# Kernel optimization log

Measured on AMD Instinct MI355X. Metric: run time of the kernel, lower is better.

The kernel has to match this reference:

```python
import jax, jax.numpy as jnp
import numpy as np

B, T, N, M, L = 128, 1024, 256, 256, 2
SCALE = 1.0 / np.sqrt(M)  # PyTorch uniform(-1/sqrt(m), 1/sqrt(m)) stdev-ish scale


def setup_inputs() -> dict:
    key = jax.random.key(0)
    ks = jax.random.split(key, 9)
    inp = {"X": jax.random.normal(ks[0], (B, T, N), dtype=jnp.float32)}
    names = ["w_ih_0", "w_hh_0", "b_ih_0", "b_hh_0", "w_ih_1", "w_hh_1", "b_ih_1", "b_hh_1"]
    shapes = [(3 * M, N), (3 * M, M), (3 * M,), (3 * M,), (3 * M, M), (3 * M, M), (3 * M,), (3 * M,)]
    for name, shp, k in zip(names, shapes, ks[1:]):
        inp[name] = jax.random.normal(k, shp, dtype=jnp.float32) * SCALE
    return inp


def _gru_layer(x, w_ih, w_hh, b_ih, b_hh):
    # x: [B, T, in] ; weights: [3m, in], [3m, m] ; gate order r, z, n (PyTorch)
    b, t, _ = x.shape
    m = w_hh.shape[1]
    gates_x = jnp.einsum('bti,gi->btg', x, w_ih) + b_ih  # [B, T, 3m], precomputed input gates

    def step(h, gx):
        gh = h @ w_hh.T + b_hh  # [B, 3m]
        r = jax.nn.sigmoid(gx[:, :m] + gh[:, :m])
        z = jax.nn.sigmoid(gx[:, m:2 * m] + gh[:, m:2 * m])
        n = jnp.tanh(gx[:, 2 * m:] + r * gh[:, 2 * m:])
        h_new = (1.0 - z) * n + z * h
        return h_new, h_new

    h0 = jnp.zeros((b, m), dtype=x.dtype)
    h_last, ys = jax.lax.scan(step, h0, jnp.swapaxes(gates_x, 0, 1))  # scan over time
    return jnp.swapaxes(ys, 0, 1), h_last  # [B, T, m], [B, m]


def reference(X, w_ih_0, w_hh_0, b_ih_0, b_hh_0, w_ih_1, w_hh_1, b_ih_1, b_hh_1):
    out0, h0 = _gru_layer(X, w_ih_0, w_hh_0, b_ih_0, b_hh_0)
    # dropout=0.0 between layers -> identity
    out1, h1 = _gru_layer(out0, w_ih_1, w_hh_1, b_ih_1, b_hh_1)
    hidden = jnp.stack([h0, h1], axis=0)  # [L, B, m] like PyTorch h_n
    return out1, hidden
```

## Files before the change

### kernel.cpp

```cpp
#include <hip/hip_runtime.h>

typedef _Float16 f16;
typedef f16   f16x8 __attribute__((ext_vector_type(8)));
typedef f16   f16x4 __attribute__((ext_vector_type(4)));
typedef float f32x4 __attribute__((ext_vector_type(4)));

#define TSEQ 1024

__device__ __forceinline__ float sigm(float x) {
    return __builtin_amdgcn_rcpf(1.0f + __expf(-x));
}
__device__ __forceinline__ float tanh_(float x) {
    return 1.0f - 2.0f * __builtin_amdgcn_rcpf(__expf(2.0f * x) + 1.0f);
}

__device__ __forceinline__ void barrier_lds() {
    asm volatile("s_waitcnt lgkmcnt(0)" ::: "memory");
    __builtin_amdgcn_s_barrier();
    asm volatile("" ::: "memory");
}

__global__ __launch_bounds__(512, 2) void gemm_gx(
    const float* __restrict__ A, const float* __restrict__ W,
    const float* __restrict__ bih, const float* __restrict__ bhh,
    f16* __restrict__ gx, int tc0, int TC)
{
    const int tid  = threadIdx.x;
    const int w    = tid >> 6;
    const int lane = tid & 63;
    const int c    = lane & 15;
    const int q    = lane >> 4;

    f16x8 wf[6][8];
    float bb[6];
#pragma unroll
    for (int k6 = 0; k6 < 6; ++k6) {
        const int g = (k6 >> 1) * 256 + w * 32 + (k6 & 1) * 16 + c;
        bb[k6] = bih[g] + (k6 < 4 ? bhh[g] : 0.f);
#pragma unroll
        for (int kk = 0; kk < 8; ++kk) {
            const float* wp = W + g * 256 + kk * 32 + q * 8;
            f32x4 w0 = *(const f32x4*)wp, w1 = *(const f32x4*)(wp + 4);
            f16x8 v;
            v[0] = (f16)w0[0]; v[1] = (f16)w0[1]; v[2] = (f16)w0[2]; v[3] = (f16)w0[3];
            v[4] = (f16)w1[0]; v[5] = (f16)w1[1]; v[6] = (f16)w1[2]; v[7] = (f16)w1[3];
            wf[k6][kk] = v;
        }
    }

    const int ntiles = TC * 8;
    for (int tile = blockIdx.x; tile < ntiles; tile += gridDim.x) {
        const int tloc = tile >> 3, wgb = tile & 7;
        const int b0 = wgb * 16, t = tc0 + tloc;

        f32x4 acc[6];
#pragma unroll
        for (int k6 = 0; k6 < 6; ++k6) acc[k6] = (f32x4){0.f, 0.f, 0.f, 0.f};

        const float* Ab = A + ((long)(b0 + c) * TSEQ + t) * 256;
#pragma unroll
        for (int kk = 0; kk < 8; ++kk) {
            f32x4 a0 = *(const f32x4*)(Ab + kk * 32 + q * 8);
            f32x4 a1 = *(const f32x4*)(Ab + kk * 32 + q * 8 + 4);
            f16x8 a;
            a[0] = (f16)a0[0]; a[1] = (f16)a0[1]; a[2] = (f16)a0[2]; a[3] = (f16)a0[3];
            a[4] = (f16)a1[0]; a[5] = (f16)a1[1]; a[6] = (f16)a1[2]; a[7] = (f16)a1[3];
#pragma unroll
            for (int k6 = 0; k6 < 6; ++k6)
                acc[k6] = __builtin_amdgcn_mfma_f32_16x16x32_f16(a, wf[k6][kk], acc[k6], 0, 0, 0);
        }

        f16* gb = gx + (long)tile * 12288;
#pragma unroll
        for (int gp = 0; gp < 3; ++gp) {
            f16x8 v;
#pragma unroll
            for (int e = 0; e < 8; ++e) {
                const int tau = e >> 2, i = e & 3;
                v[e] = (f16)(acc[gp * 2 + tau][i] + bb[gp * 2 + tau]);
            }
            *(f16x8*)(gb + w * 1536 + gp * 512 + lane * 8) = v;
        }
    }
}

__global__ __launch_bounds__(512, 2) void gru_rec(
    const f16* __restrict__ gx, const float* __restrict__ Whh,
    const float* __restrict__ bhh, float* __restrict__ hcarry,
    float* __restrict__ out, float* __restrict__ hid,
    int tc0, int TC, int first, int last)
{
    __shared__ __align__(16) float accb[3 * 256 * 12];
    __shared__ __align__(16) f16 hbuf[16 * 264];

    const int tid  = threadIdx.x;
    const int w    = tid >> 6;
    const int lane = tid & 63;
    const int c    = lane & 15;
    const int q    = lane >> 4;
    const int wgb8 = blockIdx.x;
    const int bg   = wgb8 * 8;

    const int j    = tid >> 1;
    const int half = tid & 1;

    f16x8 wf[6][8];
#pragma unroll
    for (int k6 = 0; k6 < 6; ++k6) {
        const int g = (k6 >> 1) * 256 + w * 32 + (k6 & 1) * 16 + c;
#pragma unroll
        for (int kk = 0; kk < 8; ++kk) {
            const float* wp = Whh + g * 256 + kk * 32 + q * 8;
            f32x4 w0 = *(const f32x4*)wp, w1 = *(const f32x4*)(wp + 4);
            f16x8 v;
            v[0] = (f16)w0[0]; v[1] = (f16)w0[1]; v[2] = (f16)w0[2]; v[3] = (f16)w0[3];
            v[4] = (f16)w1[0]; v[5] = (f16)w1[1]; v[6] = (f16)w1[2]; v[7] = (f16)w1[3];
            wf[k6][kk] = v;
        }
    }

    const float bbn = bhh[512 + j];

    for (int k = tid; k < 16 * 264; k += 512) hbuf[k] = (f16)0.f;
    __syncthreads();

    f16 hreg[4];
#pragma unroll
    for (int i = 0; i < 4; ++i) {
        float hv = first ? 0.f : hcarry[(long)(bg + half * 4 + i) * 256 + j];
        hreg[i] = (f16)hv;
        hbuf[(half * 4 + i) * 264 + j] = hreg[i];
    }

    const int q16   = (wgb8 & 1) * 2 + half;
    const int gxoff = (j >> 5) * 1536 + (q16 * 16 + (j & 15)) * 8 + ((j >> 4) & 1) * 4;
    const int wgb16 = wgb8 >> 1;

    f16x4 gr, gz, gn;
    {
        const f16* sl = gx + (long)wgb16 * 12288 + gxoff;
        gr = *(const f16x4*)(sl);
        gz = *(const f16x4*)(sl + 512);
        gn = *(const f16x4*)(sl + 1024);
    }
    __syncthreads();

    for (int tl = 0; tl < TC; ++tl) {
        const int t = tc0 + tl;

        const int tln = (tl + 1 < TC) ? tl + 1 : tl;
        const f16* sl = gx + ((long)tln * 8 + wgb16) * 12288 + gxoff;
        f16x4 p0 = *(const f16x4*)(sl);
        f16x4 p1 = *(const f16x4*)(sl + 512);
        f16x4 p2 = *(const f16x4*)(sl + 1024);

        f32x4 acc[6];
#pragma unroll
        for (int k6 = 0; k6 < 6; ++k6) acc[k6] = (f32x4){0.f, 0.f, 0.f, 0.f};
#pragma unroll
        for (int kk = 0; kk < 8; ++kk) {
            f16x8 a = *(const f16x8*)(hbuf + c * 264 + kk * 32 + q * 8);
#pragma unroll
            for (int k6 = 0; k6 < 6; ++k6)
                acc[k6] = __builtin_amdgcn_mfma_f32_16x16x32_f16(a, wf[k6][kk], acc[k6], 0, 0, 0);
        }

        if (q < 2) {
#pragma unroll
            for (int k6 = 0; k6 < 6; ++k6) {
                const int gp = k6 >> 1;
                const int jj = w * 32 + (k6 & 1) * 16 + c;
                *(f32x4*)(&accb[(gp * 256 + jj) * 12 + q * 4]) = acc[k6];
            }
        }

        barrier_lds();

        f32x4 ar = *(const f32x4*)(&accb[(0 * 256 + j) * 12 + half * 4]);
        f32x4 az = *(const f32x4*)(&accb[(1 * 256 + j) * 12 + half * 4]);
        f32x4 an = *(const f32x4*)(&accb[(2 * 256 + j) * 12 + half * 4]);
#pragma unroll
        for (int i = 0; i < 4; ++i) {
            float r = sigm((float)gr[i] + ar[i]);
            float z = sigm((float)gz[i] + az[i]);
            float n = tanh_((float)gn[i] + r * (an[i] + bbn));
            float hp = (float)hreg[i];
            float h = n + z * (hp - n);
            hreg[i] = (f16)h;
            hbuf[(half * 4 + i) * 264 + j] = hreg[i];
            out[((long)(bg + half * 4 + i) * TSEQ + t) * 256 + j] = h;
        }
        gr = p0; gz = p1; gn = p2;

        barrier_lds();
    }

#pragma unroll
    for (int i = 0; i < 4; ++i) {
        const long idx = (long)(bg + half * 4 + i) * 256 + j;
        hcarry[idx] = (float)hreg[i];
        if (last) hid[idx] = (float)hreg[i];
    }
}

extern "C" void kernel_launch(void* const* d_in, const int* in_sizes, int n_in,
                              void* d_out, int out_size, void* d_ws, size_t ws_size,
                              hipStream_t stream) {
    const float* X    = (const float*)d_in[0];
    const float* wih0 = (const float*)d_in[1];
    const float* whh0 = (const float*)d_in[2];
    const float* bih0 = (const float*)d_in[3];
    const float* bhh0 = (const float*)d_in[4];
    const float* wih1 = (const float*)d_in[5];
    const float* whh1 = (const float*)d_in[6];
    const float* bih1 = (const float*)d_in[7];
    const float* bhh1 = (const float*)d_in[8];

    float* out = (float*)d_out;
    float* hid = out + (long)128 * TSEQ * 256;

    float* hcarry = (float*)d_ws;
    f16*   gxws   = (f16*)((char*)d_ws + 131072);

    int TC = TSEQ;
    while (TC > 16 && (size_t)131072 + (size_t)TC * 196608 > ws_size) TC >>= 1;

    const float* wih[2] = {wih0, wih1};
    const float* whh[2] = {whh0, whh1};
    const float* bih[2] = {bih0, bih1};
    const float* bhh[2] = {bhh0, bhh1};

    for (int layer = 0; layer < 2; ++layer) {
        const float* Ain = layer ? out : X;
        for (int tc0 = 0; tc0 < TSEQ; tc0 += TC) {
            const int ntiles = TC * 8;
            const int grid = ntiles < 512 ? ntiles : 512;
            gemm_gx<<<grid, 512, 0, stream>>>(Ain, wih[layer], bih[layer], bhh[layer],
                                              gxws, tc0, TC);
            gru_rec<<<16, 512, 0, stream>>>(gxws, whh[layer], bhh[layer], hcarry,
                                            out, hid + (long)layer * 128 * 256,
                                            tc0, TC, tc0 == 0, tc0 + TC == TSEQ);
        }
    }
}
```

Before: 4.427 ms.

## Fuse GRU layers into a chunked wavefront pipeline with role-specialized blocks

Replaces the per-layer sequence of input-GEMM and recurrence launches with a single fused kernel launched once per time chunk. Within each launch, blocks take one of four roles: layer-0 recurrence, layer-1 recurrence, layer-0 input GEMM for the next chunk, or layer-1 input GEMM for the previous chunk, using double-buffered gate workspaces. This lets the layer-1 recurrence run alongside the layer-0 recurrence, shortening the serial critical path, and hides the input GEMMs behind them. The cost is more launches with smaller chunks, a larger LDS reservation per block, and reliance on kernel boundaries to order writes to the shared output buffer.

```diff
diff --git a/kernel.cpp b/kernel.cpp
--- a/kernel.cpp
+++ b/kernel.cpp
@@ -20,10 +20,9 @@
     asm volatile("" ::: "memory");
 }
 
-__global__ __launch_bounds__(512, 2) void gemm_gx(
-    const float* __restrict__ A, const float* __restrict__ W,
-    const float* __restrict__ bih, const float* __restrict__ bhh,
-    f16* __restrict__ gx, int tc0, int TC)
+__device__ void gemm_role(const float* __restrict__ A, const float* __restrict__ W,
+                          const float* __restrict__ bih, const float* __restrict__ bhh,
+                          f16* __restrict__ gxslot, int tc0, int TC, int idx, int nblk)
 {
     const int tid  = threadIdx.x;
     const int w    = tid >> 6;
@@ -49,7 +48,7 @@
     }
 
     const int ntiles = TC * 8;
-    for (int tile = blockIdx.x; tile < ntiles; tile += gridDim.x) {
+    for (int tile = idx; tile < ntiles; tile += nblk) {
         const int tloc = tile >> 3, wgb = tile & 7;
         const int b0 = wgb * 16, t = tc0 + tloc;
 
@@ -70,7 +69,7 @@
                 acc[k6] = __builtin_amdgcn_mfma_f32_16x16x32_f16(a, wf[k6][kk], acc[k6], 0, 0, 0);
         }
 
-        f16* gb = gx + (long)tile * 12288;
+        f16* gb = gxslot + (long)tile * 12288;
 #pragma unroll
         for (int gp = 0; gp < 3; ++gp) {
             f16x8 v;
@@ -84,23 +83,18 @@
     }
 }
 
-__global__ __launch_bounds__(512, 2) void gru_rec(
-    const f16* __restrict__ gx, const float* __restrict__ Whh,
-    const float* __restrict__ bhh, float* __restrict__ hcarry,
-    float* __restrict__ out, float* __restrict__ hid,
-    int tc0, int TC, int first, int last)
+__device__ void rec_role(const f16* __restrict__ gx, const float* __restrict__ Whh,
+                         const float* __restrict__ bhh, float* __restrict__ hcarry,
+                         float* out, float* __restrict__ hid,
+                         int tc0, int TC, int first, int last, int wgb8,
+                         float* accb, f16* hbuf)
 {
-    __shared__ __align__(16) float accb[3 * 256 * 12];
-    __shared__ __align__(16) f16 hbuf[16 * 264];
-
     const int tid  = threadIdx.x;
     const int w    = tid >> 6;
     const int lane = tid & 63;
     const int c    = lane & 15;
     const int q    = lane >> 4;
-    const int wgb8 = blockIdx.x;
     const int bg   = wgb8 * 8;
-
     const int j    = tid >> 1;
     const int half = tid & 1;
 
@@ -170,15 +164,15 @@
             for (int k6 = 0; k6 < 6; ++k6) {
                 const int gp = k6 >> 1;
                 const int jj = w * 32 + (k6 & 1) * 16 + c;
-                *(f32x4*)(&accb[(gp * 256 + jj) * 12 + q * 4]) = acc[k6];
+                *(f32x4*)(&accb[(gp * 256 + jj) * 8 + q * 4]) = acc[k6];
             }
         }
 
         barrier_lds();
 
-        f32x4 ar = *(const f32x4*)(&accb[(0 * 256 + j) * 12 + half * 4]);
-        f32x4 az = *(const f32x4*)(&accb[(1 * 256 + j) * 12 + half * 4]);
-        f32x4 an = *(const f32x4*)(&accb[(2 * 256 + j) * 12 + half * 4]);
+        f32x4 ar = *(const f32x4*)(&accb[(0 * 256 + j) * 8 + half * 4]);
+        f32x4 az = *(const f32x4*)(&accb[(1 * 256 + j) * 8 + half * 4]);
+        f32x4 an = *(const f32x4*)(&accb[(2 * 256 + j) * 8 + half * 4]);
 #pragma unroll
         for (int i = 0; i < 4; ++i) {
             float r = sigm((float)gr[i] + ar[i]);
@@ -200,6 +194,44 @@
         const long idx = (long)(bg + half * 4 + i) * 256 + j;
         hcarry[idx] = (float)hreg[i];
         if (last) hid[idx] = (float)hreg[i];
+    }
+}
+
+__global__ __launch_bounds__(512, 2) void fused(
+    const float* __restrict__ X,
+    const float* __restrict__ wih0, const float* __restrict__ whh0,
+    const float* __restrict__ bih0, const float* __restrict__ bhh0,
+    const float* __restrict__ wih1, const float* __restrict__ whh1,
+    const float* __restrict__ bih1, const float* __restrict__ bhh1,
+    f16* gx0, f16* gx1, float* hc0, float* hc1,
+    float* out, float* hid, int c, int TC, int C)
+{
+    __shared__ __align__(16) float accb[18432];
+    __shared__ __align__(16) f16  hbuf[16 * 264];
+
+    const long SLOT = (long)TC * 98304;
+    const int bid = blockIdx.x;
+
+    if (bid < 16) {
+        if (c >= 0 && c < C)
+            rec_role(gx0 + (long)(c & 1) * SLOT, whh0, bhh0, hc0,
+                     out, hid, c * TC, TC, c == 0, c == C - 1, bid, accb, hbuf);
+    } else if (bid < 32) {
+        const int k = c - 2;
+        if (k >= 0 && k < C)
+            rec_role(gx1 + (long)(k & 1) * SLOT, whh1, bhh1, hc1,
+                     out, hid + (long)128 * 256, k * TC, TC, k == 0, k == C - 1,
+                     bid - 16, accb, hbuf);
+    } else if (bid < 144) {
+        const int k = c + 1;
+        if (k >= 0 && k < C)
+            gemm_role(X, wih0, bih0, bhh0, gx0 + (long)(k & 1) * SLOT,
+                      k * TC, TC, bid - 32, 112);
+    } else {
+        const int k = c - 1;
+        if (k >= 0 && k < C)
+            gemm_role(out, wih1, bih1, bhh1, gx1 + (long)(k & 1) * SLOT,
+                      k * TC, TC, bid - 144, 112);
     }
 }
 
@@ -219,27 +251,17 @@
     float* out = (float*)d_out;
     float* hid = out + (long)128 * TSEQ * 256;
 
-    float* hcarry = (float*)d_ws;
-    f16*   gxws   = (f16*)((char*)d_ws + 131072);
-
-    int TC = TSEQ;
-    while (TC > 16 && (size_t)131072 + (size_t)TC * 196608 > ws_size) TC >>= 1;
-
-    const float* wih[2] = {wih0, wih1};
-    const float* whh[2] = {whh0, whh1};
-    const float* bih[2] = {bih0, bih1};
-    const float* bhh[2] = {bhh0, bhh1};
-
-    for (int layer = 0; layer < 2; ++layer) {
-        const float* Ain = layer ? out : X;
-        for (int tc0 = 0; tc0 < TSEQ; tc0 += TC) {
-            const int ntiles = TC * 8;
-            const int grid = ntiles < 512 ? ntiles : 512;
-            gemm_gx<<<grid, 512, 0, stream>>>(Ain, wih[layer], bih[layer], bhh[layer],
-                                              gxws, tc0, TC);
-            gru_rec<<<16, 512, 0, stream>>>(gxws, whh[layer], bhh[layer], hcarry,
-                                            out, hid + (long)layer * 128 * 256,
-                                            tc0, TC, tc0 == 0, tc0 + TC == TSEQ);
-        }
-    }
-}
+    int TC = 64;
+    while (TC > 4 && (size_t)262144 + (size_t)4 * TC * 196608 > ws_size) TC >>= 1;
+    const int C = TSEQ / TC;
+
+    float* hc0 = (float*)d_ws;
+    float* hc1 = hc0 + 32768;
+    f16*   gx0 = (f16*)((char*)d_ws + 262144);
+    f16*   gx1 = gx0 + (long)2 * TC * 98304;
+
+    for (int c = -1; c <= C + 1; ++c)
+        fused<<<256, 512, 0, stream>>>(X, wih0, whh0, bih0, bhh0,
+                                       wih1, whh1, bih1, bhh1,
+                                       gx0, gx1, hc0, hc1, out, hid, c, TC, C);
+}
```

Result: faster. 3.691 ms (-16.6%).
